# Kernel tuning notes

Hardware: AMD Instinct MI355X
Metric: run time of the kernel (lower is better)

Reference implementation:

```python
import jax, jax.numpy as jnp
import numpy as np

N_EMBD = 1024
N_HEAD = 16
D_HEAD = N_EMBD // N_HEAD


def setup_inputs() -> dict:
    key = jax.random.key(0)
    ks = jax.random.split(key, 5)
    x = jax.random.normal(ks[0], (4, 2048, N_EMBD), dtype=jnp.float32)
    s = 1.0 / np.sqrt(N_EMBD)
    Wq = jax.random.normal(ks[1], (N_EMBD, N_EMBD), dtype=jnp.float32) * s
    Wk = jax.random.normal(ks[2], (N_EMBD, N_EMBD), dtype=jnp.float32) * s
    Wv = jax.random.normal(ks[3], (N_EMBD, N_EMBD), dtype=jnp.float32) * s
    Wo = jax.random.normal(ks[4], (N_EMBD, N_EMBD), dtype=jnp.float32) * s
    return {"x": x, "Wq": Wq, "Wk": Wk, "Wv": Wv, "Wo": Wo}


def reference(x, Wq, Wk, Wv, Wo):
    B, S, E = x.shape
    H, Dh = N_HEAD, D_HEAD
    scale = 1.0 / np.sqrt(Dh)  # LayerwiseSDPA(d_head) -> scale by 1/sqrt(d_head)

    def proj(W):
        # nn.Linear(no bias): y = x @ W.T ; reshape to [B,H,S,Dh]
        return (x @ W.T).reshape(B, S, H, Dh).transpose(0, 2, 1, 3)

    q, k, v = proj(Wq), proj(Wk), proj(Wv)
    scores = jnp.einsum('bhsd,bhtd->bhst', q, k) * scale  # [B,H,S,S]
    causal = jnp.tril(jnp.ones((S, S), dtype=bool))
    scores = jnp.where(causal, scores, jnp.finfo(scores.dtype).min)
    attn = jax.nn.softmax(scores, axis=-1)
    y = jnp.einsum('bhst,bhtd->bhsd', attn, v)  # [B,H,S,Dh]
    y = y.transpose(0, 2, 1, 3).reshape(B, S, E)
    return y @ Wo.T
```

## Files before the change

kernel.cpp:

```cpp
#include <hip/hip_runtime.h>

typedef __bf16 bf16;
typedef bf16  bf16x8 __attribute__((ext_vector_type(8)));
typedef bf16  bf16x4 __attribute__((ext_vector_type(4)));
typedef short s16x4  __attribute__((ext_vector_type(4)));
typedef float f32x4  __attribute__((ext_vector_type(4)));

#define AS1 __attribute__((address_space(1)))
#define AS3 __attribute__((address_space(3)))

#define SQLEN 2048
#define EMB   1024

__global__ __launch_bounds__(256) void cvt_f32_bf16(const float* __restrict__ in,
                                                    bf16* __restrict__ out, int n8) {
  int i = blockIdx.x * blockDim.x + threadIdx.x;
  if (i >= n8) return;
  const float4* p = (const float4*)in + (size_t)i * 2;
  float4 a = p[0], b = p[1];
  bf16x8 o;
  o[0] = (bf16)a.x; o[1] = (bf16)a.y; o[2] = (bf16)a.z; o[3] = (bf16)a.w;
  o[4] = (bf16)b.x; o[5] = (bf16)b.y; o[6] = (bf16)b.z; o[7] = (bf16)b.w;
  *((bf16x8*)out + i) = o;
}

__global__ __launch_bounds__(256) void cvt_w4(const float* __restrict__ w0, const float* __restrict__ w1,
                                              const float* __restrict__ w2, const float* __restrict__ w3,
                                              bf16* o0, bf16* o1, bf16* o2, bf16* o3, int n8) {
  const float* in; bf16* out;
  switch (blockIdx.y) {
    case 0: in = w0; out = o0; break;
    case 1: in = w1; out = o1; break;
    case 2: in = w2; out = o2; break;
    default: in = w3; out = o3; break;
  }
  int i = blockIdx.x * blockDim.x + threadIdx.x;
  if (i >= n8) return;
  const float4* p = (const float4*)in + (size_t)i * 2;
  float4 a = p[0], b = p[1];
  bf16x8 o;
  o[0] = (bf16)a.x; o[1] = (bf16)a.y; o[2] = (bf16)a.z; o[3] = (bf16)a.w;
  o[4] = (bf16)b.x; o[5] = (bf16)b.y; o[6] = (bf16)b.z; o[7] = (bf16)b.w;
  *((bf16x8*)out + i) = o;
}

__global__ __launch_bounds__(256) void transpose_v(const bf16* __restrict__ Vb,
                                                   bf16* __restrict__ Vt) {
  __shared__ bf16 T[64][72];
  const int b = blockIdx.z;
  const int t0 = blockIdx.x * 64, n0 = blockIdx.y * 64;
  const int r = threadIdx.x >> 3, c = threadIdx.x & 7;
#pragma unroll
  for (int i = 0; i < 2; ++i) {
    const int row = i * 32 + r;
    *(bf16x8*)&T[row][c * 8] =
        *(const bf16x8*)&Vb[((size_t)(b * SQLEN + t0 + row)) * EMB + n0 + c * 8];
  }
  __syncthreads();
#pragma unroll
  for (int i = 0; i < 2; ++i) {
    const int n = i * 32 + r;
    bf16x8 o;
#pragma unroll
    for (int j = 0; j < 8; ++j) o[j] = T[c * 8 + j][n];
    *(bf16x8*)&Vt[((size_t)(b * EMB + n0 + n)) * SQLEN + t0 + c * 8] = o;
  }
}

template <int OUTF32>
__device__ __forceinline__
void gemm_body(const bf16* __restrict__ A, const bf16* __restrict__ B,
               float* __restrict__ Cf, bf16* __restrict__ Cb,
               int M, int N, int K, float scale, bf16* Asl, bf16* Bsl) {
  const int tid  = threadIdx.x;
  const int lane = tid & 63, wave = tid >> 6;
  const int quad = lane >> 4, col = lane & 15;
  const int m0 = blockIdx.x * 128, n0 = blockIdx.y * 128;
  const int wr = wave >> 1, wc = wave & 1;

  f32x4 acc[4][4];
  const f32x4 fz = {0.f, 0.f, 0.f, 0.f};
#pragma unroll
  for (int i = 0; i < 4; ++i)
#pragma unroll
    for (int j = 0; j < 4; ++j) acc[i][j] = fz;

  const int srow = lane >> 2;
  const int sk   = lane & 3;

  auto stage = [&](int buf, int k0) {
#pragma unroll
    for (int r = 0; r < 2; ++r) {
      const int c      = wave * 2 + r;
      const int row    = c * 16 + srow;
      const int gchunk = sk ^ (row & 3);
      const bf16* ga = A + (size_t)(m0 + row) * K + k0 + gchunk * 8;
      const bf16* gb = B + (size_t)(n0 + row) * K + k0 + gchunk * 8;
      __builtin_amdgcn_global_load_lds((const AS1 void*)ga, (AS3 void*)(Asl + buf * 4096 + c * 512), 16, 0, 0);
      __builtin_amdgcn_global_load_lds((const AS1 void*)gb, (AS3 void*)(Bsl + buf * 4096 + c * 512), 16, 0, 0);
    }
  };

  const int nk = K >> 5;
  stage(0, 0);
  for (int it = 0; it < nk; ++it) {
    __syncthreads();
    if (it + 1 < nk) stage((it + 1) & 1, (it + 1) << 5);
    const bf16* As = Asl + (it & 1) * 4096;
    const bf16* Bs = Bsl + (it & 1) * 4096;

    bf16x8 af[4], bfr[4];
#pragma unroll
    for (int i = 0; i < 4; ++i) {
      const int r = wr * 64 + i * 16 + col;
      af[i] = *(const bf16x8*)&As[r * 32 + ((quad ^ (col & 3)) * 8)];
    }
#pragma unroll
    for (int j = 0; j < 4; ++j) {
      const int r = wc * 64 + j * 16 + col;
      bfr[j] = *(const bf16x8*)&Bs[r * 32 + ((quad ^ (col & 3)) * 8)];
    }
#pragma unroll
    for (int i = 0; i < 4; ++i)
#pragma unroll
      for (int j = 0; j < 4; ++j)
        acc[i][j] = __builtin_amdgcn_mfma_f32_16x16x32_bf16(af[i], bfr[j], acc[i][j], 0, 0, 0);
  }

#pragma unroll
  for (int i = 0; i < 4; ++i) {
#pragma unroll
    for (int j = 0; j < 4; ++j) {
      const int gm0 = m0 + wr * 64 + i * 16 + quad * 4;
      const int gn  = n0 + wc * 64 + j * 16 + col;
#pragma unroll
      for (int r = 0; r < 4; ++r) {
        const size_t idx = (size_t)(gm0 + r) * N + gn;
        if (OUTF32) Cf[idx] = acc[i][j][r] * scale;
        else        Cb[idx] = (bf16)(acc[i][j][r] * scale);
      }
    }
  }
}

__global__ __launch_bounds__(256, 2)
void gemm_qkv(const bf16* __restrict__ A, const bf16* __restrict__ Wq,
              const bf16* __restrict__ Wk, const bf16* __restrict__ Wv,
              bf16* Qo, bf16* Ko, bf16* Vo, float qscale) {
  __shared__ bf16 Asl[2 * 4096];
  __shared__ bf16 Bsl[2 * 4096];
  const bf16* B; bf16* C; float sc = 1.0f;
  if (blockIdx.z == 0)      { B = Wq; C = Qo; sc = qscale; }
  else if (blockIdx.z == 1) { B = Wk; C = Ko; }
  else                      { B = Wv; C = Vo; }
  gemm_body<0>(A, B, nullptr, C, 8192, 1024, 1024, sc, Asl, Bsl);
}

__global__ __launch_bounds__(256, 2)
void gemm_o(const bf16* __restrict__ A, const bf16* __restrict__ W, float* __restrict__ C) {
  __shared__ bf16 Asl[2 * 4096];
  __shared__ bf16 Bsl[2 * 4096];
  gemm_body<1>(A, W, C, nullptr, 8192, 1024, 1024, 1.0f, Asl, Bsl);
}

__global__ __launch_bounds__(256, 3)
void attn_flash(const bf16* __restrict__ Q, const bf16* __restrict__ K,
                const bf16* __restrict__ Vt, bf16* __restrict__ Y) {
  __shared__ bf16 Ksb[2][64 * 64];
  __shared__ bf16 Vsb[2][64 * 64];

  const int tid  = threadIdx.x;
  const int lane = tid & 63, wave = tid >> 6;
  const int quad = lane >> 4, col = lane & 15;
  const int p  = blockIdx.x;
  const int h  = blockIdx.y;
  const int b  = blockIdx.z;
  const int hc = h * 64;
  const size_t rowBase = (size_t)b * SQLEN;

  const int srow8 = lane >> 3;
  const int sch   = lane & 7;
  const int gch   = sch ^ srow8;
  const int a7    = col & 7;

  auto stageKV = [&](int buf, int t0) {
#pragma unroll
    for (int i = 0; i < 2; ++i) {
      const int c  = wave * 2 + i;
      const int rr = c * 8 + srow8;
      const bf16* gk = K + (rowBase + t0 + rr) * EMB + hc + gch * 8;
      const bf16* gv = Vt + ((size_t)(b * EMB + hc + rr)) * SQLEN + t0 + gch * 8;
      __builtin_amdgcn_global_load_lds((const AS1 void*)gk, (AS3 void*)(&Ksb[buf][c * 512]), 16, 0, 0);
      __builtin_amdgcn_global_load_lds((const AS1 void*)gv, (AS3 void*)(&Vsb[buf][c * 512]), 16, 0, 0);
    }
  };

#pragma unroll
  for (int halfIdx = 0; halfIdx < 2; ++halfIdx) {
    const int qt = halfIdx == 0 ? (15 - p) : p;
    const int q0 = qt * 128;

    stageKV(0, 0);

    bf16x8 qf[2][2];
#pragma unroll
    for (int g = 0; g < 2; ++g) {
      const int row = g * 64 + wave * 16 + col;
      const bf16* gq = Q + (rowBase + q0 + row) * EMB + hc + quad * 8;
      qf[g][0] = *(const bf16x8*)gq;
      qf[g][1] = *(const bf16x8*)(gq + 32);
    }
    __syncthreads();

    float m_i[2] = {-INFINITY, -INFINITY}, l_i[2] = {0.f, 0.f};
    f32x4 o[2][4];
    const f32x4 fz = {0.f, 0.f, 0.f, 0.f};
#pragma unroll
    for (int g = 0; g < 2; ++g)
#pragma unroll
      for (int dd = 0; dd < 4; ++dd) o[g][dd] = fz;

    const int ntt = 2 * qt + 2;
    for (int tt = 0; tt < ntt; ++tt) {
      const int t0 = tt * 64;
      const int cur = tt & 1;
      if (tt + 1 < ntt) stageKV(cur ^ 1, t0 + 64);
      const bf16* Ks = Ksb[cur];
      const bf16* Vs = Vsb[cur];

      f32x4 s[2][4];
      __builtin_amdgcn_s_setprio(1);
#pragma unroll
      for (int sl = 0; sl < 4; ++sl) {
        const bf16x8 kf0 = *(const bf16x8*)&Ks[(sl * 16 + col) * 64 + ((quad ^ a7) * 8)];
        const bf16x8 kf1 = *(const bf16x8*)&Ks[(sl * 16 + col) * 64 + (((quad ^ 4) ^ a7) * 8)];
#pragma unroll
        for (int g = 0; g < 2; ++g) {
          f32x4 z = fz;
          z = __builtin_amdgcn_mfma_f32_16x16x32_bf16(kf0, qf[g][0], z, 0, 0, 0);
          s[g][sl] = __builtin_amdgcn_mfma_f32_16x16x32_bf16(kf1, qf[g][1], z, 0, 0, 0);
        }
      }
      __builtin_amdgcn_s_setprio(0);

      if (tt >= 2 * qt) {
#pragma unroll
        for (int g = 0; g < 2; ++g) {
          const int qg = q0 + g * 64 + wave * 16 + col;
#pragma unroll
          for (int sl = 0; sl < 4; ++sl)
#pragma unroll
            for (int r = 0; r < 4; ++r)
              if (t0 + sl * 16 + quad * 4 + r > qg) s[g][sl][r] = -INFINITY;
        }
      }

      bf16x4 pb[2][4];
#pragma unroll
      for (int g = 0; g < 2; ++g) {
        float mx = s[g][0][0];
#pragma unroll
        for (int sl = 0; sl < 4; ++sl)
#pragma unroll
          for (int r = 0; r < 4; ++r) mx = fmaxf(mx, s[g][sl][r]);
        mx = fmaxf(mx, __shfl_xor(mx, 16));
        mx = fmaxf(mx, __shfl_xor(mx, 32));
        if (!__all(mx <= m_i[g] + 8.f)) {
          const float mnew = fmaxf(m_i[g], mx);
          const float a = __builtin_amdgcn_exp2f(m_i[g] - mnew);
          l_i[g] *= a;
#pragma unroll
          for (int dd = 0; dd < 4; ++dd) o[g][dd] *= a;
          m_i[g] = mnew;
        }
        float rs = 0.f;
#pragma unroll
        for (int sl = 0; sl < 4; ++sl)
#pragma unroll
          for (int r = 0; r < 4; ++r) {
            const float pv = __builtin_amdgcn_exp2f(s[g][sl][r] - m_i[g]);
            rs += pv;
            pb[g][sl][r] = (bf16)pv;
          }
        rs += __shfl_xor(rs, 16);
        rs += __shfl_xor(rs, 32);
        l_i[g] += rs;
      }

      __builtin_amdgcn_s_setprio(1);
#pragma unroll
      for (int sl = 0; sl < 4; ++sl) {
        const s16x4 pf0 = __builtin_bit_cast(s16x4, pb[0][sl]);
        const s16x4 pf1 = __builtin_bit_cast(s16x4, pb[1][sl]);
        const int cch  = 2 * sl + (quad >> 1);
        const int half = quad & 1;
#pragma unroll
        for (int dd = 0; dd < 4; ++dd) {
          const int row = dd * 16 + col;
          const bf16x4 vb = *(const bf16x4*)&Vs[row * 64 + ((cch ^ a7) * 8) + half * 4];
          const s16x4 vf = __builtin_bit_cast(s16x4, vb);
          o[0][dd] = __builtin_amdgcn_mfma_f32_16x16x16bf16_1k(vf, pf0, o[0][dd], 0, 0, 0);
          o[1][dd] = __builtin_amdgcn_mfma_f32_16x16x16bf16_1k(vf, pf1, o[1][dd], 0, 0, 0);
        }
      }
      __builtin_amdgcn_s_setprio(0);
      __syncthreads();
    }

    bf16* Ot = &Ksb[0][0] + wave * 1280;
#pragma unroll
    for (int g = 0; g < 2; ++g) {
      const float rl = __builtin_amdgcn_rcpf(l_i[g]);
#pragma unroll
      for (int dd = 0; dd < 4; ++dd) {
        bf16x4 ob;
#pragma unroll
        for (int r = 0; r < 4; ++r) ob[r] = (bf16)(o[g][dd][r] * rl);
        *(bf16x4*)&Ot[col * 72 + dd * 16 + quad * 4] = ob;
      }
#pragma unroll
      for (int i = 0; i < 2; ++i) {
        const int row = i * 8 + srow8;
        const bf16x8 v = *(const bf16x8*)&Ot[row * 72 + sch * 8];
        *(bf16x8*)&Y[(rowBase + q0 + g * 64 + wave * 16 + row) * EMB + hc + sch * 8] = v;
      }
    }
    if (halfIdx == 0) __syncthreads();
  }
}

extern "C" void kernel_launch(void* const* d_in, const int* in_sizes, int n_in,
                              void* d_out, int out_size, void* d_ws, size_t ws_size,
                              hipStream_t stream) {
  const float* x  = (const float*)d_in[0];
  const float* Wq = (const float*)d_in[1];
  const float* Wk = (const float*)d_in[2];
  const float* Wv = (const float*)d_in[3];
  const float* Wo = (const float*)d_in[4];
  float* out = (float*)d_out;

  const size_t ME = 8192ull * 1024ull;
  const size_t WE = 1024ull * 1024ull;
  bf16* ws  = (bf16*)d_ws;
  bf16* xb  = ws;
  bf16* wqb = xb + ME;
  bf16* wkb = wqb + WE;
  bf16* wvb = wkb + WE;
  bf16* wob = wvb + WE;
  bf16* Qb  = wob + WE;
  bf16* Kb  = Qb + ME;
  bf16* Vb  = Kb + ME;
  bf16* Yb  = Vb + ME;
  bf16* Vtb = xb;

  cvt_f32_bf16<<<(int)(ME / 8 / 256), 256, 0, stream>>>(x, xb, (int)(ME / 8));
  cvt_w4<<<dim3((int)(WE / 8 / 256), 4), 256, 0, stream>>>(Wq, Wk, Wv, Wo, wqb, wkb, wvb, wob, (int)(WE / 8));

  const float qscale = 0.125f * 1.4426950408889634f;
  gemm_qkv<<<dim3(64, 8, 3), 256, 0, stream>>>(xb, wqb, wkb, wvb, Qb, Kb, Vb, qscale);

  transpose_v<<<dim3(32, 16, 4), 256, 0, stream>>>(Vb, Vtb);
  attn_flash<<<dim3(8, 16, 4), 256, 0, stream>>>(Qb, Kb, Vtb, Yb);

  gemm_o<<<dim3(64, 8), 256, 0, stream>>>(Yb, wob, out);
}
```

Baseline: 266.2 us.

## Fuse V transpose into QKV GEMM epilogue and use 8-wave attention blocks

The QKV GEMM now writes V directly in transposed [B,E,S] layout from its epilogue, which removes the separate transpose kernel and its extra global round trip. The flash attention kernel moves to 512 threads, with each wave handling 16 query rows instead of 32. This halves per-wave registers and K/V staging work, and raises the number of waves per block to share LDS tiles. The trade-offs are that the transposed epilogue writes 8-byte scattered stores with strided addresses, and the attention kernel does more syncs and LDS reads per FLOP.

```diff
diff --git a/kernel.cpp b/kernel.cpp
--- a/kernel.cpp
+++ b/kernel.cpp
@@ -44,34 +44,11 @@
   *((bf16x8*)out + i) = o;
 }
 
-__global__ __launch_bounds__(256) void transpose_v(const bf16* __restrict__ Vb,
-                                                   bf16* __restrict__ Vt) {
-  __shared__ bf16 T[64][72];
-  const int b = blockIdx.z;
-  const int t0 = blockIdx.x * 64, n0 = blockIdx.y * 64;
-  const int r = threadIdx.x >> 3, c = threadIdx.x & 7;
-#pragma unroll
-  for (int i = 0; i < 2; ++i) {
-    const int row = i * 32 + r;
-    *(bf16x8*)&T[row][c * 8] =
-        *(const bf16x8*)&Vb[((size_t)(b * SQLEN + t0 + row)) * EMB + n0 + c * 8];
-  }
-  __syncthreads();
-#pragma unroll
-  for (int i = 0; i < 2; ++i) {
-    const int n = i * 32 + r;
-    bf16x8 o;
-#pragma unroll
-    for (int j = 0; j < 8; ++j) o[j] = T[c * 8 + j][n];
-    *(bf16x8*)&Vt[((size_t)(b * EMB + n0 + n)) * SQLEN + t0 + c * 8] = o;
-  }
-}
-
 template <int OUTF32>
 __device__ __forceinline__
 void gemm_body(const bf16* __restrict__ A, const bf16* __restrict__ B,
                float* __restrict__ Cf, bf16* __restrict__ Cb,
-               int M, int N, int K, float scale, bf16* Asl, bf16* Bsl) {
+               int M, int N, int K, float scale, bf16* Asl, bf16* Bsl, int vtr) {
   const int tid  = threadIdx.x;
   const int lane = tid & 63, wave = tid >> 6;
   const int quad = lane >> 4, col = lane & 15;
@@ -133,11 +110,21 @@
     for (int j = 0; j < 4; ++j) {
       const int gm0 = m0 + wr * 64 + i * 16 + quad * 4;
       const int gn  = n0 + wc * 64 + j * 16 + col;
-#pragma unroll
-      for (int r = 0; r < 4; ++r) {
-        const size_t idx = (size_t)(gm0 + r) * N + gn;
-        if (OUTF32) Cf[idx] = acc[i][j][r] * scale;
-        else        Cb[idx] = (bf16)(acc[i][j][r] * scale);
+      if (OUTF32) {
+#pragma unroll
+        for (int r = 0; r < 4; ++r)
+          Cf[(size_t)(gm0 + r) * N + gn] = acc[i][j][r] * scale;
+      } else if (vtr) {
+        bf16x4 ob;
+#pragma unroll
+        for (int r = 0; r < 4; ++r) ob[r] = (bf16)(acc[i][j][r] * scale);
+        const int bb = gm0 >> 11;
+        const int t_ = gm0 & 2047;
+        *(bf16x4*)&Cb[((size_t)(bb * 1024 + gn)) * 2048 + t_] = ob;
+      } else {
+#pragma unroll
+        for (int r = 0; r < 4; ++r)
+          Cb[(size_t)(gm0 + r) * N + gn] = (bf16)(acc[i][j][r] * scale);
       }
     }
   }
@@ -146,28 +133,29 @@
 __global__ __launch_bounds__(256, 2)
 void gemm_qkv(const bf16* __restrict__ A, const bf16* __restrict__ Wq,
               const bf16* __restrict__ Wk, const bf16* __restrict__ Wv,
-              bf16* Qo, bf16* Ko, bf16* Vo, float qscale) {
+              bf16* Qo, bf16* Ko, bf16* Vto, float qscale) {
   __shared__ bf16 Asl[2 * 4096];
   __shared__ bf16 Bsl[2 * 4096];
-  const bf16* B; bf16* C; float sc = 1.0f;
+  const bf16* B; bf16* C; float sc = 1.0f; int vtr = 0;
   if (blockIdx.z == 0)      { B = Wq; C = Qo; sc = qscale; }
   else if (blockIdx.z == 1) { B = Wk; C = Ko; }
-  else                      { B = Wv; C = Vo; }
-  gemm_body<0>(A, B, nullptr, C, 8192, 1024, 1024, sc, Asl, Bsl);
+  else                      { B = Wv; C = Vto; vtr = 1; }
+  gemm_body<0>(A, B, nullptr, C, 8192, 1024, 1024, sc, Asl, Bsl, vtr);
 }
 
 __global__ __launch_bounds__(256, 2)
 void gemm_o(const bf16* __restrict__ A, const bf16* __restrict__ W, float* __restrict__ C) {
   __shared__ bf16 Asl[2 * 4096];
   __shared__ bf16 Bsl[2 * 4096];
-  gemm_body<1>(A, W, C, nullptr, 8192, 1024, 1024, 1.0f, Asl, Bsl);
-}
-
-__global__ __launch_bounds__(256, 3)
+  gemm_body<1>(A, W, C, nullptr, 8192, 1024, 1024, 1.0f, Asl, Bsl, 0);
+}
+
+__global__ __launch_bounds__(512, 4)
 void attn_flash(const bf16* __restrict__ Q, const bf16* __restrict__ K,
                 const bf16* __restrict__ Vt, bf16* __restrict__ Y) {
-  __shared__ bf16 Ksb[2][64 * 64];
-  __shared__ bf16 Vsb[2][64 * 64];
+  __shared__ bf16 smem[4 * 4096];
+  bf16* Ksb0 = smem;
+  bf16* Vsb0 = smem + 2 * 4096;
 
   const int tid  = threadIdx.x;
   const int lane = tid & 63, wave = tid >> 6;
@@ -184,15 +172,12 @@
   const int a7    = col & 7;
 
   auto stageKV = [&](int buf, int t0) {
-#pragma unroll
-    for (int i = 0; i < 2; ++i) {
-      const int c  = wave * 2 + i;
-      const int rr = c * 8 + srow8;
-      const bf16* gk = K + (rowBase + t0 + rr) * EMB + hc + gch * 8;
-      const bf16* gv = Vt + ((size_t)(b * EMB + hc + rr)) * SQLEN + t0 + gch * 8;
-      __builtin_amdgcn_global_load_lds((const AS1 void*)gk, (AS3 void*)(&Ksb[buf][c * 512]), 16, 0, 0);
-      __builtin_amdgcn_global_load_lds((const AS1 void*)gv, (AS3 void*)(&Vsb[buf][c * 512]), 16, 0, 0);
-    }
+    const int c  = wave;
+    const int rr = c * 8 + srow8;
+    const bf16* gk = K + (rowBase + t0 + rr) * EMB + hc + gch * 8;
+    const bf16* gv = Vt + ((size_t)(b * EMB + hc + rr)) * SQLEN + t0 + gch * 8;
+    __builtin_amdgcn_global_load_lds((const AS1 void*)gk, (AS3 void*)(Ksb0 + buf * 4096 + c * 512), 16, 0, 0);
+    __builtin_amdgcn_global_load_lds((const AS1 void*)gv, (AS3 void*)(Vsb0 + buf * 4096 + c * 512), 16, 0, 0);
   };
 
 #pragma unroll
@@ -202,96 +187,85 @@
 
     stageKV(0, 0);
 
-    bf16x8 qf[2][2];
-#pragma unroll
-    for (int g = 0; g < 2; ++g) {
-      const int row = g * 64 + wave * 16 + col;
+    bf16x8 qf0, qf1;
+    {
+      const int row = wave * 16 + col;
       const bf16* gq = Q + (rowBase + q0 + row) * EMB + hc + quad * 8;
-      qf[g][0] = *(const bf16x8*)gq;
-      qf[g][1] = *(const bf16x8*)(gq + 32);
+      qf0 = *(const bf16x8*)gq;
+      qf1 = *(const bf16x8*)(gq + 32);
     }
     __syncthreads();
 
-    float m_i[2] = {-INFINITY, -INFINITY}, l_i[2] = {0.f, 0.f};
-    f32x4 o[2][4];
+    float m_i = -INFINITY, l_i = 0.f;
+    f32x4 o[4];
     const f32x4 fz = {0.f, 0.f, 0.f, 0.f};
 #pragma unroll
-    for (int g = 0; g < 2; ++g)
-#pragma unroll
-      for (int dd = 0; dd < 4; ++dd) o[g][dd] = fz;
+    for (int dd = 0; dd < 4; ++dd) o[dd] = fz;
 
     const int ntt = 2 * qt + 2;
     for (int tt = 0; tt < ntt; ++tt) {
       const int t0 = tt * 64;
       const int cur = tt & 1;
       if (tt + 1 < ntt) stageKV(cur ^ 1, t0 + 64);
-      const bf16* Ks = Ksb[cur];
-      const bf16* Vs = Vsb[cur];
-
-      f32x4 s[2][4];
+      const bf16* Ks = Ksb0 + cur * 4096;
+      const bf16* Vs = Vsb0 + cur * 4096;
+
+      f32x4 s[4];
       __builtin_amdgcn_s_setprio(1);
 #pragma unroll
       for (int sl = 0; sl < 4; ++sl) {
         const bf16x8 kf0 = *(const bf16x8*)&Ks[(sl * 16 + col) * 64 + ((quad ^ a7) * 8)];
         const bf16x8 kf1 = *(const bf16x8*)&Ks[(sl * 16 + col) * 64 + (((quad ^ 4) ^ a7) * 8)];
-#pragma unroll
-        for (int g = 0; g < 2; ++g) {
-          f32x4 z = fz;
-          z = __builtin_amdgcn_mfma_f32_16x16x32_bf16(kf0, qf[g][0], z, 0, 0, 0);
-          s[g][sl] = __builtin_amdgcn_mfma_f32_16x16x32_bf16(kf1, qf[g][1], z, 0, 0, 0);
-        }
+        f32x4 z = fz;
+        z = __builtin_amdgcn_mfma_f32_16x16x32_bf16(kf0, qf0, z, 0, 0, 0);
+        s[sl] = __builtin_amdgcn_mfma_f32_16x16x32_bf16(kf1, qf1, z, 0, 0, 0);
       }
       __builtin_amdgcn_s_setprio(0);
 
       if (tt >= 2 * qt) {
-#pragma unroll
-        for (int g = 0; g < 2; ++g) {
-          const int qg = q0 + g * 64 + wave * 16 + col;
-#pragma unroll
-          for (int sl = 0; sl < 4; ++sl)
-#pragma unroll
-            for (int r = 0; r < 4; ++r)
-              if (t0 + sl * 16 + quad * 4 + r > qg) s[g][sl][r] = -INFINITY;
-        }
-      }
-
-      bf16x4 pb[2][4];
-#pragma unroll
-      for (int g = 0; g < 2; ++g) {
-        float mx = s[g][0][0];
+        const int qg = q0 + wave * 16 + col;
 #pragma unroll
         for (int sl = 0; sl < 4; ++sl)
 #pragma unroll
-          for (int r = 0; r < 4; ++r) mx = fmaxf(mx, s[g][sl][r]);
+          for (int r = 0; r < 4; ++r)
+            if (t0 + sl * 16 + quad * 4 + r > qg) s[sl][r] = -INFINITY;
+      }
+
+      bf16x4 pb[4];
+      {
+        float mx = s[0][0];
+#pragma unroll
+        for (int sl = 0; sl < 4; ++sl)
+#pragma unroll
+          for (int r = 0; r < 4; ++r) mx = fmaxf(mx, s[sl][r]);
         mx = fmaxf(mx, __shfl_xor(mx, 16));
         mx = fmaxf(mx, __shfl_xor(mx, 32));
-        if (!__all(mx <= m_i[g] + 8.f)) {
-          const float mnew = fmaxf(m_i[g], mx);
-          const float a = __builtin_amdgcn_exp2f(m_i[g] - mnew);
-          l_i[g] *= a;
-#pragma unroll
-          for (int dd = 0; dd < 4; ++dd) o[g][dd] *= a;
-          m_i[g] = mnew;
+        if (!__all(mx <= m_i + 8.f)) {
+          const float mnew = fmaxf(m_i, mx);
+          const float a = __builtin_amdgcn_exp2f(m_i - mnew);
+          l_i *= a;
+#pragma unroll
+          for (int dd = 0; dd < 4; ++dd) o[dd] *= a;
+          m_i = mnew;
         }
         float rs = 0.f;
 #pragma unroll
         for (int sl = 0; sl < 4; ++sl)
 #pragma unroll
           for (int r = 0; r < 4; ++r) {
-            const float pv = __builtin_amdgcn_exp2f(s[g][sl][r] - m_i[g]);
+            const float pv = __builtin_amdgcn_exp2f(s[sl][r] - m_i);
             rs += pv;
-            pb[g][sl][r] = (bf16)pv;
+            pb[sl][r] = (bf16)pv;
           }
         rs += __shfl_xor(rs, 16);
         rs += __shfl_xor(rs, 32);
-        l_i[g] += rs;
+        l_i += rs;
       }
 
       __builtin_amdgcn_s_setprio(1);
 #pragma unroll
       for (int sl = 0; sl < 4; ++sl) {
-        const s16x4 pf0 = __builtin_bit_cast(s16x4, pb[0][sl]);
-        const s16x4 pf1 = __builtin_bit_cast(s16x4, pb[1][sl]);
+        const s16x4 pf = __builtin_bit_cast(s16x4, pb[sl]);
         const int cch  = 2 * sl + (quad >> 1);
         const int half = quad & 1;
 #pragma unroll
@@ -299,30 +273,28 @@
           const int row = dd * 16 + col;
           const bf16x4 vb = *(const bf16x4*)&Vs[row * 64 + ((cch ^ a7) * 8) + half * 4];
           const s16x4 vf = __builtin_bit_cast(s16x4, vb);
-          o[0][dd] = __builtin_amdgcn_mfma_f32_16x16x16bf16_1k(vf, pf0, o[0][dd], 0, 0, 0);
-          o[1][dd] = __builtin_amdgcn_mfma_f32_16x16x16bf16_1k(vf, pf1, o[1][dd], 0, 0, 0);
+          o[dd] = __builtin_amdgcn_mfma_f32_16x16x16bf16_1k(vf, pf, o[dd], 0, 0, 0);
         }
       }
       __builtin_amdgcn_s_setprio(0);
       __syncthreads();
     }
 
-    bf16* Ot = &Ksb[0][0] + wave * 1280;
-#pragma unroll
-    for (int g = 0; g < 2; ++g) {
-      const float rl = __builtin_amdgcn_rcpf(l_i[g]);
+    bf16* Ot = smem + wave * 1152;
+    {
+      const float rl = __builtin_amdgcn_rcpf(l_i);
 #pragma unroll
       for (int dd = 0; dd < 4; ++dd) {
         bf16x4 ob;
 #pragma unroll
-        for (int r = 0; r < 4; ++r) ob[r] = (bf16)(o[g][dd][r] * rl);
+        for (int r = 0; r < 4; ++r) ob[r] = (bf16)(o[dd][r] * rl);
         *(bf16x4*)&Ot[col * 72 + dd * 16 + quad * 4] = ob;
       }
 #pragma unroll
       for (int i = 0; i < 2; ++i) {
         const int row = i * 8 + srow8;
         const bf16x8 v = *(const bf16x8*)&Ot[row * 72 + sch * 8];
-        *(bf16x8*)&Y[(rowBase + q0 + g * 64 + wave * 16 + row) * EMB + hc + sch * 8] = v;
+        *(bf16x8*)&Y[(rowBase + q0 + wave * 16 + row) * EMB + hc + sch * 8] = v;
       }
     }
     if (halfIdx == 0) __syncthreads();
@@ -349,18 +321,16 @@
   bf16* wob = wvb + WE;
   bf16* Qb  = wob + WE;
   bf16* Kb  = Qb + ME;
-  bf16* Vb  = Kb + ME;
-  bf16* Yb  = Vb + ME;
-  bf16* Vtb = xb;
+  bf16* Vtb = Kb + ME;
+  bf16* Yb  = Vtb + ME;
 
   cvt_f32_bf16<<<(int)(ME / 8 / 256), 256, 0, stream>>>(x, xb, (int)(ME / 8));
   cvt_w4<<<dim3((int)(WE / 8 / 256), 4), 256, 0, stream>>>(Wq, Wk, Wv, Wo, wqb, wkb, wvb, wob, (int)(WE / 8));
 
   const float qscale = 0.125f * 1.4426950408889634f;
-  gemm_qkv<<<dim3(64, 8, 3), 256, 0, stream>>>(xb, wqb, wkb, wvb, Qb, Kb, Vb, qscale);
-
-  transpose_v<<<dim3(32, 16, 4), 256, 0, stream>>>(Vb, Vtb);
-  attn_flash<<<dim3(8, 16, 4), 256, 0, stream>>>(Qb, Kb, Vtb, Yb);
+  gemm_qkv<<<dim3(64, 8, 3), 256, 0, stream>>>(xb, wqb, wkb, wvb, Qb, Kb, Vtb, qscale);
+
+  attn_flash<<<dim3(8, 16, 4), 512, 0, stream>>>(Qb, Kb, Vtb, Yb);
 
   gemm_o<<<dim3(64, 8), 256, 0, stream>>>(Yb, wob, out);
 }
```

Result: faster. 257.8 us (-3.2%).
